# Performance work log

Hardware: AMD Instinct MI355X
Metric: run time of the kernel (lower is better)

The kernel has to match this reference:

```python
import jax, jax.numpy as jnp
import numpy as np

NUM_HEADS = 8
NUM_GROUPS = 32
EPS = 1e-5
RESCALE = 1.0


def setup_inputs() -> dict:
    key = jax.random.key(0)
    ks = jax.random.split(key, 7)
    b, c, h, w = 16, 512, 32, 32
    return {
        "x": jax.random.normal(ks[0], (b, c, h, w), jnp.float32),
        "norm_w": jax.random.normal(ks[1], (c,), jnp.float32),
        "norm_b": jax.random.normal(ks[2], (c,), jnp.float32),
        "qkv_w": jax.random.normal(ks[3], (3 * c, c), jnp.float32) * (c ** -0.5),
        "qkv_b": jax.random.normal(ks[4], (3 * c,), jnp.float32) * 0.02,
        "proj_w": jax.random.normal(ks[5], (c, c), jnp.float32) * (c ** -0.5),
        "proj_b": jax.random.normal(ks[6], (c,), jnp.float32) * 0.02,
    }


def _group_norm(x, w, b):
    # x: [B, C, L]
    B, C, L = x.shape
    g = x.reshape(B, NUM_GROUPS, (C // NUM_GROUPS) * L)
    mu = jnp.mean(g, axis=-1, keepdims=True)
    var = jnp.var(g, axis=-1, keepdims=True)
    g = (g - mu) * jax.lax.rsqrt(var + EPS)
    return g.reshape(B, C, L) * w[None, :, None] + b[None, :, None]


def reference(x, norm_w, norm_b, qkv_w, qkv_b, proj_w, proj_b):
    b, c, hh, ww = x.shape
    L = hh * ww
    H = NUM_HEADS
    ch = c // H  # head dim

    xr = x.reshape(b, c, L)
    hid = _group_norm(xr, norm_w, norm_b)

    # 1x1 conv1d == matmul over channel dim: [3c, c] @ [b, c, L]
    qkv = jnp.einsum('oc,bcl->bol', qkv_w, hid) + qkv_b[None, :, None]
    # torch: reshape(b*H, 3*ch, L).split(ch) -> per-head contiguous [q|k|v] blocks
    qkv = qkv.reshape(b, H, 3, ch, L)
    q, k, v = qkv[:, :, 0], qkv[:, :, 1], qkv[:, :, 2]  # [b, H, ch, L]

    scale = 1.0 / (ch ** 0.25)
    weight = jnp.einsum('bhct,bhcs->bhts', q * scale, k * scale)
    weight = jax.nn.softmax(weight.astype(jnp.float32), axis=-1).astype(weight.dtype)
    a = jnp.einsum('bhts,bhcs->bhct', weight, v)  # [b, H, ch, L]

    h = a.reshape(b, c, L)
    h = jnp.einsum('oc,bcl->bol', proj_w, h) + proj_b[None, :, None]
    h = h.reshape(b, c, hh, ww)
    return (x + h) / RESCALE
```

## Files before the change

### kernel.cpp

```cpp
#include <hip/hip_runtime.h>
#include <hip/hip_bf16.h>
#include <stdint.h>


using f32x4  = __attribute__((ext_vector_type(4))) float;
using bf16x8 = __attribute__((ext_vector_type(8))) __bf16;
using s8v    = __attribute__((ext_vector_type(8))) short;
using s4v    = __attribute__((ext_vector_type(4))) short;

__device__ __forceinline__ short f2bf(float f){
  union { float f; unsigned u; } c; c.f = f;
  unsigned r = (c.u + 0x7FFFu + ((c.u >> 16) & 1u)) >> 16;
  return (short)r;
}

__device__ __forceinline__ float exp2_fast(float x){
#if __has_builtin(__builtin_amdgcn_exp2f)
  return __builtin_amdgcn_exp2f(x);
#else
  return exp2f(x);
#endif
}

__device__ __forceinline__ void gl_lds16(const void* g, void* l){
  __builtin_amdgcn_global_load_lds((const __attribute__((address_space(1))) void*)g,
                                   (__attribute__((address_space(3))) void*)l, 16, 0, 0);
}

__global__ __launch_bounds__(256) void k_pre(const float* __restrict__ x,
                                             const float* __restrict__ w,
                                             const float* __restrict__ bia,
                                             short* __restrict__ hid,
                                             const float* __restrict__ qw,
                                             const float* __restrict__ pw,
                                             const float* __restrict__ qb,
                                             short* __restrict__ qwb,
                                             short* __restrict__ pwb,
                                             float* __restrict__ qbp){
  int bid = blockIdx.x;
  int tid = threadIdx.x;
  if (bid >= 512){
    int i = (bid - 512) * 256 + tid;
    if (i < 786432){
      int o = i >> 9, kk = i & 511;
      int h = o / 192, rem = o - h*192;
      int nr = (rem >> 6)*512 + h*64 + (rem & 63);
      qwb[nr*512 + kk] = f2bf(qw[i]);
    } else if (i < 1048576){
      int j = i - 786432;
      pwb[j] = f2bf(pw[j]);
    } else if (i < 1050112){
      int o = i - 1048576;
      int h = o / 192, rem = o - h*192;
      qbp[(rem >> 6)*512 + h*64 + (rem & 63)] = qb[o];
    }
    return;
  }
  int b = bid >> 5;
  int g = bid & 31;
  const float* xg = x + ((size_t)b*512 + g*16)*1024;
  int l0 = tid * 4;
  float v[16][4];
  float s1 = 0.f, s2 = 0.f;
  #pragma unroll
  for (int c = 0; c < 16; c++){
    f32x4 t = *(const f32x4*)(xg + c*1024 + l0);
    #pragma unroll
    for (int j = 0; j < 4; j++){ v[c][j] = t[j]; s1 += t[j]; s2 += t[j]*t[j]; }
  }
  #pragma unroll
  for (int m = 32; m; m >>= 1){ s1 += __shfl_xor(s1, m); s2 += __shfl_xor(s2, m); }
  __shared__ float r1[4], r2[4];
  int wv = tid >> 6, ln = tid & 63;
  if (ln == 0){ r1[wv] = s1; r2[wv] = s2; }
  __syncthreads();
  s1 = r1[0]+r1[1]+r1[2]+r1[3];
  s2 = r2[0]+r2[1]+r2[2]+r2[3];
  float mu = s1 * (1.f/16384.f);
  float var = s2 * (1.f/16384.f) - mu*mu;
  float rs = rsqrtf(var + 1e-5f);
  float ww[16], bb[16];
  #pragma unroll
  for (int c = 0; c < 16; c++){ ww[c] = w[g*16+c]*rs; bb[c] = bia[g*16+c]; }
  #pragma unroll
  for (int j = 0; j < 4; j++){
    short o[16];
    #pragma unroll
    for (int c = 0; c < 16; c++) o[c] = f2bf((v[c][j]-mu)*ww[c] + bb[c]);
    short* dst = hid + ((size_t)(b*1024 + l0 + j))*512 + g*16;
    *(s8v*)dst     = *(s8v*)o;
    *(s8v*)(dst+8) = *(s8v*)(o+8);
  }
}

__global__ __launch_bounds__(256) void k_gemmQ(
    const short* __restrict__ A, const short* __restrict__ Bm,
    const float* __restrict__ bias,
    short* __restrict__ q_t, short* __restrict__ k_t, short* __restrict__ v_t)
{
  __shared__ short Al[2][128*64];
  __shared__ short Bl[2][128*64];
  int id = blockIdx.x;
  int xcd = id & 7, ix = id >> 3;
  int mt = ix % 12, nt = ix / 12;
  int m0 = mt * 128;
  int n0 = (xcd + 8*nt) * 128;
  int tid = threadIdx.x;
  int lane = tid & 63;
  int wv = tid >> 6;
  int wr = wv >> 1, wc = wv & 1;
  int l15 = lane & 15, g = lane >> 4;
  f32x4 acc[4][4] = {};

  const short* srcp[8]; char* dstp[8];
  #pragma unroll
  for (int i = 0; i < 8; i++){
    int cc = wv*8 + i;
    if (cc < 16){
      int slot = cc*64 + lane;
      int row = slot >> 3, off = slot & 7;
      srcp[i] = A + (size_t)(m0+row)*512 + (off ^ (row&7))*8;
      dstp[i] = (char*)Al[0] + cc*1024;
    } else {
      int slot = (cc-16)*64 + lane;
      int row = slot >> 3, off = slot & 7;
      srcp[i] = Bm + (size_t)(n0+row)*512 + (off ^ (row&7))*8;
      dstp[i] = (char*)Bl[0] + (cc-16)*1024;
    }
  }

  auto STAGE = [&](int db, int t){
    #pragma unroll
    for (int i = 0; i < 8; i++)
      gl_lds16(srcp[i] + t*64, dstp[i] + db*16384);
  };

  auto COMPUTE = [&](int db){
    #pragma unroll
    for (int kk = 0; kk < 2; kk++){
      bf16x8 af[4], bf[4];
      #pragma unroll
      for (int m = 0; m < 4; m++){
        int row = wr*64 + m*16 + l15;
        int byte = row*128 + (((kk*64) + (g*16)) ^ ((row&7)<<4));
        af[m] = *(const bf16x8*)((char*)Al[db] + byte);
      }
      #pragma unroll
      for (int n = 0; n < 4; n++){
        int row = wc*64 + n*16 + l15;
        int byte = row*128 + (((kk*64) + (g*16)) ^ ((row&7)<<4));
        bf[n] = *(const bf16x8*)((char*)Bl[db] + byte);
      }
      __builtin_amdgcn_s_setprio(1);
      #pragma unroll
      for (int m = 0; m < 4; m++)
        #pragma unroll
        for (int n = 0; n < 4; n++)
          acc[m][n] = __builtin_amdgcn_mfma_f32_16x16x32_bf16(af[m], bf[n], acc[m][n], 0, 0, 0);
      __builtin_amdgcn_s_setprio(0);
    }
  };

  STAGE(0, 0);
  for (int t = 0; t < 8; t++){
    __syncthreads();
    if (t < 7) STAGE((t+1)&1, t+1);
    COMPUTE(t&1);
  }
  __syncthreads();

  int sel = m0 >> 9;
  if (sel < 2){
    const float sc = (sel == 0) ? 0.18033688011112042f : 1.0f;
    short* dstb = (sel == 0) ? q_t : k_t;
    #pragma unroll
    for (int m = 0; m < 4; m++){
      int ob = m0 + wr*64 + m*16 + (g<<2);
      int hh = (ob>>6)&7, c0 = ob&63;
      float bs[4];
      #pragma unroll
      for (int r = 0; r < 4; r++) bs[r] = bias[ob+r];
      #pragma unroll
      for (int n = 0; n < 4; n++){
        int nn = n0 + wc*64 + n*16 + l15;
        int bb = nn >> 10, ll = nn & 1023;
        int bh = bb*8 + hh;
        short o4[4];
        #pragma unroll
        for (int r = 0; r < 4; r++) o4[r] = f2bf((acc[m][n][r] + bs[r]) * sc);
        *(s4v*)(dstb + ((size_t)bh*1024 + ll)*64 + c0) = *(s4v*)o4;
      }
    }
  } else {
    short* Sc = (short*)Al;
    #pragma unroll
    for (int m = 0; m < 4; m++){
      int ob = m0 + wr*64 + m*16 + (g<<2);
      int h2 = (ob>>6)&1, cq = (ob>>4)&3;
      float bs[4];
      #pragma unroll
      for (int r = 0; r < 4; r++) bs[r] = bias[ob+r];
      #pragma unroll
      for (int n = 0; n < 4; n++){
        int nn = n0 + wc*64 + n*16 + l15;
        int sl = nn & 63, sreg = (nn>>6)&1;
        int ks2 = sl >> 5, gq = (sl>>2)&3, i2 = (sl&3) + 4*((sl>>4)&1);
        int base = (h2*2 + sreg)*4096 + (((ks2*4+gq)*4 + cq)*16 + (g<<2))*8 + i2;
        #pragma unroll
        for (int r = 0; r < 4; r++)
          Sc[base + r*8] = f2bf(acc[m][n][r] + bs[r]);
      }
    }
    __syncthreads();
    int b0  = n0 >> 10;
    int s64 = (n0 >> 6) & 15;
    int hb  = (m0 - 1024) >> 6;
    #pragma unroll
    for (int it = 0; it < 8; it++){
      int flat = it*2048 + tid*8;
      int h2 = flat >> 13, rem = flat & 8191, sreg = rem >> 12, off = rem & 4095;
      int bh = b0*8 + hb + h2;
      *(s8v*)(v_t + ((size_t)bh*16 + s64 + sreg)*4096 + off) = *(const s8v*)(Sc + flat);
    }
  }
}

__global__ __launch_bounds__(256) void k_gemmP(
    const short* __restrict__ A, const short* __restrict__ Bm,
    const float* __restrict__ bias, const float* __restrict__ xres,
    float* __restrict__ outp)
{
  __shared__ short Al[2][128*64];
  __shared__ short Bl[2][128*64];
  int id = blockIdx.x;
  int xcd = id & 7, ix = id >> 3;
  int mt = ix & 3, nt = ix >> 2;
  int m0 = mt * 128;
  int n0 = (xcd + 8*nt) * 128;
  int tid = threadIdx.x;
  int lane = tid & 63;
  int wv = tid >> 6;
  int wr = wv >> 1, wc = wv & 1;
  int l15 = lane & 15, g = lane >> 4;
  f32x4 acc[4][4] = {};

  const short* srcp[8]; char* dstp[8];
  #pragma unroll
  for (int i = 0; i < 8; i++){
    int cc = wv*8 + i;
    if (cc < 16){
      int slot = cc*64 + lane;
      int row = slot >> 3, off = slot & 7;
      srcp[i] = A + (size_t)(m0+row)*512 + (off ^ (row&7))*8;
      dstp[i] = (char*)Al[0] + cc*1024;
    } else {
      int slot = (cc-16)*64 + lane;
      int row = slot >> 3, off = slot & 7;
      srcp[i] = Bm + (size_t)(n0+row)*512 + (off ^ (row&7))*8;
      dstp[i] = (char*)Bl[0] + (cc-16)*1024;
    }
  }

  auto STAGE = [&](int db, int t){
    #pragma unroll
    for (int i = 0; i < 8; i++)
      gl_lds16(srcp[i] + t*64, dstp[i] + db*16384);
  };

  auto COMPUTE = [&](int db){
    #pragma unroll
    for (int kk = 0; kk < 2; kk++){
      bf16x8 af[4], bf[4];
      #pragma unroll
      for (int m = 0; m < 4; m++){
        int row = wr*64 + m*16 + l15;
        int byte = row*128 + (((kk*64) + (g*16)) ^ ((row&7)<<4));
        af[m] = *(const bf16x8*)((char*)Al[db] + byte);
      }
      #pragma unroll
      for (int n = 0; n < 4; n++){
        int row = wc*64 + n*16 + l15;
        int byte = row*128 + (((kk*64) + (g*16)) ^ ((row&7)<<4));
        bf[n] = *(const bf16x8*)((char*)Bl[db] + byte);
      }
      __builtin_amdgcn_s_setprio(1);
      #pragma unroll
      for (int m = 0; m < 4; m++)
        #pragma unroll
        for (int n = 0; n < 4; n++)
          acc[m][n] = __builtin_amdgcn_mfma_f32_16x16x32_bf16(af[m], bf[n], acc[m][n], 0, 0, 0);
      __builtin_amdgcn_s_setprio(0);
    }
  };

  STAGE(0, 0);
  for (int t = 0; t < 8; t++){
    __syncthreads();
    if (t < 7) STAGE((t+1)&1, t+1);
    COMPUTE(t&1);
  }

  #pragma unroll
  for (int m = 0; m < 4; m++){
    int ob = m0 + wr*64 + m*16 + (g<<2);
    float bs[4];
    #pragma unroll
    for (int r = 0; r < 4; r++) bs[r] = bias[ob+r];
    #pragma unroll
    for (int n = 0; n < 4; n++){
      int nn = n0 + wc*64 + n*16 + l15;
      int bb = nn >> 10, ll = nn & 1023;
      #pragma unroll
      for (int r = 0; r < 4; r++){
        size_t idx = ((size_t)bb*512 + ob + r)*1024 + ll;
        outp[idx] = xres[idx] + acc[m][n][r] + bs[r];
      }
    }
  }
}

__global__ __launch_bounds__(256, 4) void k_attn(
    const short* __restrict__ q_t, const short* __restrict__ k_t,
    const short* __restrict__ v_t, short* __restrict__ a_bt)
{
  __shared__ short Kh[4*2048];
  __shared__ short Vh[4*2048];
  int id = blockIdx.x;
  int xcd = id & 7, ix = id >> 3;
  int bh = xcd*16 + (ix >> 3);
  int qb = ix & 7;
  int bb = bh >> 3, hh = bh & 7;
  int tid = threadIdx.x;
  int lane = tid & 63;
  int wv = tid >> 6;
  int l15 = lane & 15, g = lane >> 4;

  bf16x8 qf[2][2];
  #pragma unroll
  for (int qt = 0; qt < 2; qt++){
    const short* qbase = q_t + ((size_t)bh*1024 + qb*128 + qt*64 + wv*16 + l15)*64 + g*8;
    qf[qt][0] = *(const bf16x8*)(qbase);
    qf[qt][1] = *(const bf16x8*)(qbase + 32);
  }
  asm volatile("" :: "v"(qf[0][0]), "v"(qf[0][1]), "v"(qf[1][0]), "v"(qf[1][1]));

  bf16x8 onesb;
  #pragma unroll
  for (int i = 0; i < 8; i++) onesb[i] = (__bf16)1.0f;

  f32x4 o[2][4] = {};
  f32x4 osum[2] = {};

  const short* sp[2]; char* dp[2];
  #pragma unroll
  for (int i = 0; i < 2; i++){
    int cc = wv*2 + i;
    if (cc < 4){
      int row = cc*8 + (lane>>3), slot = lane & 7;
      sp[i] = k_t + ((size_t)bh*1024 + row)*64 + (slot ^ (row&7))*8;
      dp[i] = (char*)Kh + cc*1024;
    } else {
      sp[i] = v_t + (size_t)bh*16*4096 + (cc-4)*512 + lane*8;
      dp[i] = (char*)Vh + (cc-4)*1024;
    }
  }
  auto STAGE = [&](int db, int h){
    #pragma unroll
    for (int i = 0; i < 2; i++)
      gl_lds16(sp[i] + h*2048, dp[i] + db*4096);
  };

  auto QK = [&](f32x4 (&scl)[2][2], int db){
    const char* Kb = (const char*)Kh + db*4096;
    #pragma unroll
    for (int qt = 0; qt < 2; qt++)
      #pragma unroll
      for (int jl = 0; jl < 2; jl++)
        scl[qt][jl] = f32x4{0.f, 0.f, 0.f, 0.f};
    #pragma unroll
    for (int jl = 0; jl < 2; jl++){
      int row = jl*16 + l15;
      int swz = (row&7)<<4;
      bf16x8 kf0 = *(const bf16x8*)(Kb + row*128 + ((g*16) ^ swz));
      bf16x8 kf1 = *(const bf16x8*)(Kb + row*128 + ((64 + g*16) ^ swz));
      __builtin_amdgcn_s_setprio(1);
      #pragma unroll
      for (int qt = 0; qt < 2; qt++){
        scl[qt][jl] = __builtin_amdgcn_mfma_f32_16x16x32_bf16(kf0, qf[qt][0], scl[qt][jl], 0, 0, 0);
        scl[qt][jl] = __builtin_amdgcn_mfma_f32_16x16x32_bf16(kf1, qf[qt][1], scl[qt][jl], 0, 0, 0);
      }
      __builtin_amdgcn_s_setprio(0);
    }
  };

  auto EXP_PV = [&](f32x4 (&scl)[2][2], int db){
    const char* Vb = (const char*)Vh + db*4096;
    bf16x8 pa[2];
    #pragma unroll
    for (int qt = 0; qt < 2; qt++){
      #pragma unroll
      for (int i2 = 0; i2 < 8; i2++)
        pa[qt][i2] = (__bf16)exp2_fast(scl[qt][i2>>2][i2&3]);
      osum[qt] = __builtin_amdgcn_mfma_f32_16x16x32_bf16(pa[qt], onesb, osum[qt], 0, 0, 0);
    }
    #pragma unroll
    for (int jd = 0; jd < 4; jd++){
      bf16x8 vbb = *(const bf16x8*)(Vb + (g*4+jd)*256 + l15*16);
      __builtin_amdgcn_s_setprio(1);
      #pragma unroll
      for (int qt = 0; qt < 2; qt++)
        o[qt][jd] = __builtin_amdgcn_mfma_f32_16x16x32_bf16(pa[qt], vbb, o[qt][jd], 0, 0, 0);
      __builtin_amdgcn_s_setprio(0);
    }
  };

  f32x4 sA[2][2], sB[2][2];

  STAGE(0, 0);
  STAGE(1, 1);
  asm volatile("s_waitcnt vmcnt(2)" ::: "memory");
  __builtin_amdgcn_s_barrier();
  __builtin_amdgcn_sched_barrier(0);
  QK(sA, 0);
  for (int h = 0; h < 30; h += 2){
    STAGE((h+2)&3, h+2);
    asm volatile("s_waitcnt vmcnt(2)" ::: "memory");
    __builtin_amdgcn_s_barrier();
    __builtin_amdgcn_sched_barrier(0);
    QK(sB, (h+1)&3);
    EXP_PV(sA, h&3);
    STAGE((h+3)&3, h+3);
    asm volatile("s_waitcnt vmcnt(2)" ::: "memory");
    __builtin_amdgcn_s_barrier();
    __builtin_amdgcn_sched_barrier(0);
    QK(sA, (h+2)&3);
    EXP_PV(sB, (h+1)&3);
  }
  asm volatile("s_waitcnt vmcnt(0)" ::: "memory");
  __builtin_amdgcn_s_barrier();
  __builtin_amdgcn_sched_barrier(0);
  QK(sB, 3);
  EXP_PV(sA, 2);
  EXP_PV(sB, 3);

  #pragma unroll
  for (int qt = 0; qt < 2; qt++){
    #pragma unroll
    for (int r = 0; r < 4; r++){
      float inv = 1.f / osum[qt][r];
      int qrow = qb*128 + qt*64 + wv*16 + g*4 + r;
      #pragma unroll
      for (int jd = 0; jd < 4; jd++)
        a_bt[((size_t)bb*1024 + qrow)*512 + hh*64 + jd*16 + l15] = f2bf(o[qt][jd][r] * inv);
    }
  }
}

extern "C" void kernel_launch(void* const* d_in, const int* in_sizes, int n_in,
                              void* d_out, int out_size, void* d_ws, size_t ws_size,
                              hipStream_t stream){
  const float* x  = (const float*)d_in[0];
  const float* nw = (const float*)d_in[1];
  const float* nb = (const float*)d_in[2];
  const float* qw = (const float*)d_in[3];
  const float* qb = (const float*)d_in[4];
  const float* pw = (const float*)d_in[5];
  const float* pb = (const float*)d_in[6];
  float* outp = (float*)d_out;

  char* ws = (char*)d_ws;
  short* hid  = (short*)(ws);
  short* qwb  = (short*)(ws + 16777216);
  short* pwb  = (short*)(ws + 18350080);
  short* q_t  = (short*)(ws + 18874368);
  short* k_t  = (short*)(ws + 35651584);
  short* v_t  = (short*)(ws + 52428800);
  short* a_bt = hid;
  float* qbp  = (float*)d_out;
  if (ws_size < 69206016) return;

  k_pre<<<4615, 256, 0, stream>>>(x, nw, nb, hid, qw, pw, qb, qwb, pwb, qbp);
  k_gemmQ<<<1536, 256, 0, stream>>>(qwb, hid, qbp, q_t, k_t, v_t);
  k_attn<<<1024, 256, 0, stream>>>(q_t, k_t, v_t, a_bt);
  k_gemmP<<<512, 256, 0, stream>>>(pwb, a_bt, pb, x, outp);
}
```

Baseline: 115.3 us.

## Switch attention kernel to 32x32x16 MFMA tiles with matching V layout

The attention kernel now uses 32x32x16 bf16 MFMA instructions instead of 16x16x32. Each wave handles 32 query rows against 32 keys per step, and the V staging layout written by the QKV GEMM epilogue is permuted to match the new operand fragment order. This is meant to cut the MFMA instruction count and the LDS fragment loads per step. In exchange it changes the accumulator register layout and the output row mapping, which risks register pressure and less even interleaving of exp and MFMA work.

```diff
diff --git a/kernel.cpp b/kernel.cpp
--- a/kernel.cpp
+++ b/kernel.cpp
@@ -4,6 +4,7 @@
 
 
 using f32x4  = __attribute__((ext_vector_type(4))) float;
+using f32x16 = __attribute__((ext_vector_type(16))) float;
 using bf16x8 = __attribute__((ext_vector_type(8))) __bf16;
 using s8v    = __attribute__((ext_vector_type(8))) short;
 using s4v    = __attribute__((ext_vector_type(4))) short;
@@ -196,7 +197,9 @@
     #pragma unroll
     for (int m = 0; m < 4; m++){
       int ob = m0 + wr*64 + m*16 + (g<<2);
-      int h2 = (ob>>6)&1, cq = (ob>>4)&3;
+      int h2 = (ob>>6)&1;
+      int dbase = ob & 63;
+      int dh = dbase >> 5, dl = dbase & 31;
       float bs[4];
       #pragma unroll
       for (int r = 0; r < 4; r++) bs[r] = bias[ob+r];
@@ -204,8 +207,10 @@
       for (int n = 0; n < 4; n++){
         int nn = n0 + wc*64 + n*16 + l15;
         int sl = nn & 63, sreg = (nn>>6)&1;
-        int ks2 = sl >> 5, gq = (sl>>2)&3, i2 = (sl&3) + 4*((sl>>4)&1);
-        int base = (h2*2 + sreg)*4096 + (((ks2*4+gq)*4 + cq)*16 + (g<<2))*8 + i2;
+        int ks2 = sl >> 5, s32 = sl & 31;
+        int c = s32 >> 4, s16 = s32 & 15;
+        int hc = (s16 >> 2) & 1, e = (s16 & 3) + 4*(s16 >> 3);
+        int base = (h2*2 + sreg)*4096 + ks2*2048 + (((c*2 + dh)*2 + hc)*32 + dl)*8 + e;
         #pragma unroll
         for (int r = 0; r < 4; r++)
           Sc[base + r*8] = f2bf(acc[m][n][r] + bs[r]);
@@ -333,23 +338,24 @@
   int tid = threadIdx.x;
   int lane = tid & 63;
   int wv = tid >> 6;
-  int l15 = lane & 15, g = lane >> 4;
-
-  bf16x8 qf[2][2];
-  #pragma unroll
-  for (int qt = 0; qt < 2; qt++){
-    const short* qbase = q_t + ((size_t)bh*1024 + qb*128 + qt*64 + wv*16 + l15)*64 + g*8;
-    qf[qt][0] = *(const bf16x8*)(qbase);
-    qf[qt][1] = *(const bf16x8*)(qbase + 32);
-  }
-  asm volatile("" :: "v"(qf[0][0]), "v"(qf[0][1]), "v"(qf[1][0]), "v"(qf[1][1]));
+  int l31 = lane & 31, h = lane >> 5;
+
+  bf16x8 qf[4];
+  {
+    const short* qbase = q_t + ((size_t)bh*1024 + qb*128 + wv*32 + l31)*64 + h*8;
+    qf[0] = *(const bf16x8*)(qbase);
+    qf[1] = *(const bf16x8*)(qbase + 16);
+    qf[2] = *(const bf16x8*)(qbase + 32);
+    qf[3] = *(const bf16x8*)(qbase + 48);
+  }
+  asm volatile("" :: "v"(qf[0]), "v"(qf[1]), "v"(qf[2]), "v"(qf[3]));
 
   bf16x8 onesb;
   #pragma unroll
   for (int i = 0; i < 8; i++) onesb[i] = (__bf16)1.0f;
 
-  f32x4 o[2][4] = {};
-  f32x4 osum[2] = {};
+  f32x16 o0 = {}, o1 = {};
+  f32x16 osum = {};
 
   const short* sp[2]; char* dp[2];
   #pragma unroll
@@ -364,57 +370,48 @@
       dp[i] = (char*)Vh + (cc-4)*1024;
     }
   }
-  auto STAGE = [&](int db, int h){
+  auto STAGE = [&](int db, int hf){
     #pragma unroll
     for (int i = 0; i < 2; i++)
-      gl_lds16(sp[i] + h*2048, dp[i] + db*4096);
-  };
-
-  auto QK = [&](f32x4 (&scl)[2][2], int db){
+      gl_lds16(sp[i] + hf*2048, dp[i] + db*4096);
+  };
+
+  auto QK = [&](f32x16& sc, int db){
     const char* Kb = (const char*)Kh + db*4096;
-    #pragma unroll
-    for (int qt = 0; qt < 2; qt++)
-      #pragma unroll
-      for (int jl = 0; jl < 2; jl++)
-        scl[qt][jl] = f32x4{0.f, 0.f, 0.f, 0.f};
-    #pragma unroll
-    for (int jl = 0; jl < 2; jl++){
-      int row = jl*16 + l15;
-      int swz = (row&7)<<4;
-      bf16x8 kf0 = *(const bf16x8*)(Kb + row*128 + ((g*16) ^ swz));
-      bf16x8 kf1 = *(const bf16x8*)(Kb + row*128 + ((64 + g*16) ^ swz));
-      __builtin_amdgcn_s_setprio(1);
-      #pragma unroll
-      for (int qt = 0; qt < 2; qt++){
-        scl[qt][jl] = __builtin_amdgcn_mfma_f32_16x16x32_bf16(kf0, qf[qt][0], scl[qt][jl], 0, 0, 0);
-        scl[qt][jl] = __builtin_amdgcn_mfma_f32_16x16x32_bf16(kf1, qf[qt][1], scl[qt][jl], 0, 0, 0);
-      }
-      __builtin_amdgcn_s_setprio(0);
-    }
-  };
-
-  auto EXP_PV = [&](f32x4 (&scl)[2][2], int db){
+    sc = f32x16{};
+    __builtin_amdgcn_s_setprio(1);
+    #pragma unroll
+    for (int d0 = 0; d0 < 4; d0++){
+      int byte = l31*128 + (((d0*32) + h*16) ^ ((l31&7)<<4));
+      bf16x8 kf = *(const bf16x8*)(Kb + byte);
+      sc = __builtin_amdgcn_mfma_f32_32x32x16_bf16(kf, qf[d0], sc, 0, 0, 0);
+    }
+    __builtin_amdgcn_s_setprio(0);
+  };
+
+  auto EXP_PV = [&](f32x16& sc, int db){
     const char* Vb = (const char*)Vh + db*4096;
-    bf16x8 pa[2];
-    #pragma unroll
-    for (int qt = 0; qt < 2; qt++){
-      #pragma unroll
-      for (int i2 = 0; i2 < 8; i2++)
-        pa[qt][i2] = (__bf16)exp2_fast(scl[qt][i2>>2][i2&3]);
-      osum[qt] = __builtin_amdgcn_mfma_f32_16x16x32_bf16(pa[qt], onesb, osum[qt], 0, 0, 0);
-    }
-    #pragma unroll
-    for (int jd = 0; jd < 4; jd++){
-      bf16x8 vbb = *(const bf16x8*)(Vb + (g*4+jd)*256 + l15*16);
-      __builtin_amdgcn_s_setprio(1);
-      #pragma unroll
-      for (int qt = 0; qt < 2; qt++)
-        o[qt][jd] = __builtin_amdgcn_mfma_f32_16x16x32_bf16(pa[qt], vbb, o[qt][jd], 0, 0, 0);
-      __builtin_amdgcn_s_setprio(0);
-    }
-  };
-
-  f32x4 sA[2][2], sB[2][2];
+    bf16x8 pa0, pa1;
+    #pragma unroll
+    for (int e = 0; e < 8; e++){
+      pa0[e] = (__bf16)exp2_fast(sc[e]);
+      pa1[e] = (__bf16)exp2_fast(sc[8+e]);
+    }
+    osum = __builtin_amdgcn_mfma_f32_32x32x16_bf16(pa0, onesb, osum, 0, 0, 0);
+    osum = __builtin_amdgcn_mfma_f32_32x32x16_bf16(pa1, onesb, osum, 0, 0, 0);
+    bf16x8 v00 = *(const bf16x8*)(Vb + (0*2+h)*512 + l31*16);
+    bf16x8 v01 = *(const bf16x8*)(Vb + (2   +h)*512 + l31*16);
+    bf16x8 v10 = *(const bf16x8*)(Vb + (4   +h)*512 + l31*16);
+    bf16x8 v11 = *(const bf16x8*)(Vb + (6   +h)*512 + l31*16);
+    __builtin_amdgcn_s_setprio(1);
+    o0 = __builtin_amdgcn_mfma_f32_32x32x16_bf16(pa0, v00, o0, 0, 0, 0);
+    o0 = __builtin_amdgcn_mfma_f32_32x32x16_bf16(pa1, v10, o0, 0, 0, 0);
+    o1 = __builtin_amdgcn_mfma_f32_32x32x16_bf16(pa0, v01, o1, 0, 0, 0);
+    o1 = __builtin_amdgcn_mfma_f32_32x32x16_bf16(pa1, v11, o1, 0, 0, 0);
+    __builtin_amdgcn_s_setprio(0);
+  };
+
+  f32x16 sA, sB;
 
   STAGE(0, 0);
   STAGE(1, 1);
@@ -422,19 +419,19 @@
   __builtin_amdgcn_s_barrier();
   __builtin_amdgcn_sched_barrier(0);
   QK(sA, 0);
-  for (int h = 0; h < 30; h += 2){
-    STAGE((h+2)&3, h+2);
+  for (int hf = 0; hf < 30; hf += 2){
+    STAGE((hf+2)&3, hf+2);
     asm volatile("s_waitcnt vmcnt(2)" ::: "memory");
     __builtin_amdgcn_s_barrier();
     __builtin_amdgcn_sched_barrier(0);
-    QK(sB, (h+1)&3);
-    EXP_PV(sA, h&3);
-    STAGE((h+3)&3, h+3);
+    QK(sB, (hf+1)&3);
+    EXP_PV(sA, hf&3);
+    STAGE((hf+3)&3, hf+3);
     asm volatile("s_waitcnt vmcnt(2)" ::: "memory");
     __builtin_amdgcn_s_barrier();
     __builtin_amdgcn_sched_barrier(0);
-    QK(sA, (h+2)&3);
-    EXP_PV(sB, (h+1)&3);
+    QK(sA, (hf+2)&3);
+    EXP_PV(sB, (hf+1)&3);
   }
   asm volatile("s_waitcnt vmcnt(0)" ::: "memory");
   __builtin_amdgcn_s_barrier();
@@ -444,15 +441,12 @@
   EXP_PV(sB, 3);
 
   #pragma unroll
-  for (int qt = 0; qt < 2; qt++){
-    #pragma unroll
-    for (int r = 0; r < 4; r++){
-      float inv = 1.f / osum[qt][r];
-      int qrow = qb*128 + qt*64 + wv*16 + g*4 + r;
-      #pragma unroll
-      for (int jd = 0; jd < 4; jd++)
-        a_bt[((size_t)bb*1024 + qrow)*512 + hh*64 + jd*16 + l15] = f2bf(o[qt][jd][r] * inv);
-    }
+  for (int r = 0; r < 16; r++){
+    float inv = 1.f / osum[r];
+    int qrow = qb*128 + wv*32 + (r&3) + 8*(r>>2) + 4*h;
+    size_t base = ((size_t)bb*1024 + qrow)*512 + hh*64;
+    a_bt[base + l31]      = f2bf(o0[r] * inv);
+    a_bt[base + 32 + l31] = f2bf(o1[r] * inv);
   }
 }
 
```

Result: slower. 119.0 us (+3.3%).

## Triple-buffer GEMM K-loop with 32-wide K tiles and explicit vmcnt waits

Applied to the files above, without the earlier changes.

Both the QKV and projection GEMM kernels move from a double-buffered loop over 64-wide K tiles to a triple-buffered loop over 32-wide K tiles. Loads run two stages ahead, and each step waits with s_waitcnt vmcnt instead of a full __syncthreads. The LDS swizzle is reworked for 64-byte rows. The aim is to hide global-to-LDS latency better while keeping the LDS footprint the same (48KB), at the cost of twice as many barrier iterations and less MFMA work per step. The waitcnt counts rely on how the compiler places the async loads.

```diff
diff --git a/kernel.cpp b/kernel.cpp
--- a/kernel.cpp
+++ b/kernel.cpp
@@ -98,8 +98,7 @@
     const float* __restrict__ bias,
     short* __restrict__ q_t, short* __restrict__ k_t, short* __restrict__ v_t)
 {
-  __shared__ short Al[2][128*64];
-  __shared__ short Bl[2][128*64];
+  __shared__ short Lds[3*8192];
   int id = blockIdx.x;
   int xcd = id & 7, ix = id >> 3;
   int mt = ix % 12, nt = ix / 12;
@@ -112,60 +111,60 @@
   int l15 = lane & 15, g = lane >> 4;
   f32x4 acc[4][4] = {};
 
-  const short* srcp[8]; char* dstp[8];
-  #pragma unroll
-  for (int i = 0; i < 8; i++){
-    int cc = wv*8 + i;
-    if (cc < 16){
-      int slot = cc*64 + lane;
-      int row = slot >> 3, off = slot & 7;
-      srcp[i] = A + (size_t)(m0+row)*512 + (off ^ (row&7))*8;
-      dstp[i] = (char*)Al[0] + cc*1024;
+  const short* srcp[4]; char* dstp[4];
+  #pragma unroll
+  for (int i = 0; i < 4; i++){
+    int cc = wv*4 + i;
+    int c2 = cc & 7;
+    int row = c2*16 + (lane>>2), slot = lane & 3;
+    if (cc < 8){
+      srcp[i] = A + (size_t)(m0+row)*512 + ((slot ^ ((row>>1)&3))*8);
+      dstp[i] = (char*)Lds + c2*1024;
     } else {
-      int slot = (cc-16)*64 + lane;
-      int row = slot >> 3, off = slot & 7;
-      srcp[i] = Bm + (size_t)(n0+row)*512 + (off ^ (row&7))*8;
-      dstp[i] = (char*)Bl[0] + (cc-16)*1024;
-    }
-  }
-
-  auto STAGE = [&](int db, int t){
-    #pragma unroll
-    for (int i = 0; i < 8; i++)
-      gl_lds16(srcp[i] + t*64, dstp[i] + db*16384);
-  };
-
-  auto COMPUTE = [&](int db){
-    #pragma unroll
-    for (int kk = 0; kk < 2; kk++){
-      bf16x8 af[4], bf[4];
-      #pragma unroll
-      for (int m = 0; m < 4; m++){
-        int row = wr*64 + m*16 + l15;
-        int byte = row*128 + (((kk*64) + (g*16)) ^ ((row&7)<<4));
-        af[m] = *(const bf16x8*)((char*)Al[db] + byte);
-      }
-      #pragma unroll
-      for (int n = 0; n < 4; n++){
-        int row = wc*64 + n*16 + l15;
-        int byte = row*128 + (((kk*64) + (g*16)) ^ ((row&7)<<4));
-        bf[n] = *(const bf16x8*)((char*)Bl[db] + byte);
-      }
-      __builtin_amdgcn_s_setprio(1);
-      #pragma unroll
-      for (int m = 0; m < 4; m++)
-        #pragma unroll
-        for (int n = 0; n < 4; n++)
-          acc[m][n] = __builtin_amdgcn_mfma_f32_16x16x32_bf16(af[m], bf[n], acc[m][n], 0, 0, 0);
-      __builtin_amdgcn_s_setprio(0);
-    }
+      srcp[i] = Bm + (size_t)(n0+row)*512 + ((slot ^ ((row>>1)&3))*8);
+      dstp[i] = (char*)Lds + 8192 + c2*1024;
+    }
+  }
+
+  auto STAGE = [&](int b, int t){
+    #pragma unroll
+    for (int i = 0; i < 4; i++)
+      gl_lds16(srcp[i] + t*32, dstp[i] + b*16384);
+  };
+
+  auto COMPUTE = [&](int b){
+    const char* Ab = (const char*)Lds + b*16384;
+    const char* Bb = Ab + 8192;
+    bf16x8 af[4], bf[4];
+    #pragma unroll
+    for (int m = 0; m < 4; m++){
+      int row = wr*64 + m*16 + l15;
+      af[m] = *(const bf16x8*)(Ab + row*64 + ((g*16) ^ (((row>>1)&3)<<4)));
+    }
+    #pragma unroll
+    for (int n = 0; n < 4; n++){
+      int row = wc*64 + n*16 + l15;
+      bf[n] = *(const bf16x8*)(Bb + row*64 + ((g*16) ^ (((row>>1)&3)<<4)));
+    }
+    __builtin_amdgcn_s_setprio(1);
+    #pragma unroll
+    for (int m = 0; m < 4; m++)
+      #pragma unroll
+      for (int n = 0; n < 4; n++)
+        acc[m][n] = __builtin_amdgcn_mfma_f32_16x16x32_bf16(af[m], bf[n], acc[m][n], 0, 0, 0);
+    __builtin_amdgcn_s_setprio(0);
   };
 
   STAGE(0, 0);
-  for (int t = 0; t < 8; t++){
-    __syncthreads();
-    if (t < 7) STAGE((t+1)&1, t+1);
-    COMPUTE(t&1);
+  STAGE(1, 1);
+  #pragma unroll
+  for (int t = 0; t < 16; t++){
+    if (t < 15) asm volatile("s_waitcnt vmcnt(4)" ::: "memory");
+    else        asm volatile("s_waitcnt vmcnt(0)" ::: "memory");
+    __builtin_amdgcn_s_barrier();
+    __builtin_amdgcn_sched_barrier(0);
+    if (t < 14) STAGE((t+2)%3, t+2);
+    COMPUTE(t%3);
   }
   __syncthreads();
 
@@ -192,7 +191,7 @@
       }
     }
   } else {
-    short* Sc = (short*)Al;
+    short* Sc = Lds;
     #pragma unroll
     for (int m = 0; m < 4; m++){
       int ob = m0 + wr*64 + m*16 + (g<<2);
@@ -230,8 +229,7 @@
     const float* __restrict__ bias, const float* __restrict__ xres,
     float* __restrict__ outp)
 {
-  __shared__ short Al[2][128*64];
-  __shared__ short Bl[2][128*64];
+  __shared__ short Lds[3*8192];
   int id = blockIdx.x;
   int xcd = id & 7, ix = id >> 3;
   int mt = ix & 3, nt = ix >> 2;
@@ -244,60 +242,60 @@
   int l15 = lane & 15, g = lane >> 4;
   f32x4 acc[4][4] = {};
 
-  const short* srcp[8]; char* dstp[8];
-  #pragma unroll
-  for (int i = 0; i < 8; i++){
-    int cc = wv*8 + i;
-    if (cc < 16){
-      int slot = cc*64 + lane;
-      int row = slot >> 3, off = slot & 7;
-      srcp[i] = A + (size_t)(m0+row)*512 + (off ^ (row&7))*8;
-      dstp[i] = (char*)Al[0] + cc*1024;
+  const short* srcp[4]; char* dstp[4];
+  #pragma unroll
+  for (int i = 0; i < 4; i++){
+    int cc = wv*4 + i;
+    int c2 = cc & 7;
+    int row = c2*16 + (lane>>2), slot = lane & 3;
+    if (cc < 8){
+      srcp[i] = A + (size_t)(m0+row)*512 + ((slot ^ ((row>>1)&3))*8);
+      dstp[i] = (char*)Lds + c2*1024;
     } else {
-      int slot = (cc-16)*64 + lane;
-      int row = slot >> 3, off = slot & 7;
-      srcp[i] = Bm + (size_t)(n0+row)*512 + (off ^ (row&7))*8;
-      dstp[i] = (char*)Bl[0] + (cc-16)*1024;
-    }
-  }
-
-  auto STAGE = [&](int db, int t){
-    #pragma unroll
-    for (int i = 0; i < 8; i++)
-      gl_lds16(srcp[i] + t*64, dstp[i] + db*16384);
-  };
-
-  auto COMPUTE = [&](int db){
-    #pragma unroll
-    for (int kk = 0; kk < 2; kk++){
-      bf16x8 af[4], bf[4];
-      #pragma unroll
-      for (int m = 0; m < 4; m++){
-        int row = wr*64 + m*16 + l15;
-        int byte = row*128 + (((kk*64) + (g*16)) ^ ((row&7)<<4));
-        af[m] = *(const bf16x8*)((char*)Al[db] + byte);
-      }
-      #pragma unroll
-      for (int n = 0; n < 4; n++){
-        int row = wc*64 + n*16 + l15;
-        int byte = row*128 + (((kk*64) + (g*16)) ^ ((row&7)<<4));
-        bf[n] = *(const bf16x8*)((char*)Bl[db] + byte);
-      }
-      __builtin_amdgcn_s_setprio(1);
-      #pragma unroll
-      for (int m = 0; m < 4; m++)
-        #pragma unroll
-        for (int n = 0; n < 4; n++)
-          acc[m][n] = __builtin_amdgcn_mfma_f32_16x16x32_bf16(af[m], bf[n], acc[m][n], 0, 0, 0);
-      __builtin_amdgcn_s_setprio(0);
-    }
+      srcp[i] = Bm + (size_t)(n0+row)*512 + ((slot ^ ((row>>1)&3))*8);
+      dstp[i] = (char*)Lds + 8192 + c2*1024;
+    }
+  }
+
+  auto STAGE = [&](int b, int t){
+    #pragma unroll
+    for (int i = 0; i < 4; i++)
+      gl_lds16(srcp[i] + t*32, dstp[i] + b*16384);
+  };
+
+  auto COMPUTE = [&](int b){
+    const char* Ab = (const char*)Lds + b*16384;
+    const char* Bb = Ab + 8192;
+    bf16x8 af[4], bf[4];
+    #pragma unroll
+    for (int m = 0; m < 4; m++){
+      int row = wr*64 + m*16 + l15;
+      af[m] = *(const bf16x8*)(Ab + row*64 + ((g*16) ^ (((row>>1)&3)<<4)));
+    }
+    #pragma unroll
+    for (int n = 0; n < 4; n++){
+      int row = wc*64 + n*16 + l15;
+      bf[n] = *(const bf16x8*)(Bb + row*64 + ((g*16) ^ (((row>>1)&3)<<4)));
+    }
+    __builtin_amdgcn_s_setprio(1);
+    #pragma unroll
+    for (int m = 0; m < 4; m++)
+      #pragma unroll
+      for (int n = 0; n < 4; n++)
+        acc[m][n] = __builtin_amdgcn_mfma_f32_16x16x32_bf16(af[m], bf[n], acc[m][n], 0, 0, 0);
+    __builtin_amdgcn_s_setprio(0);
   };
 
   STAGE(0, 0);
-  for (int t = 0; t < 8; t++){
-    __syncthreads();
-    if (t < 7) STAGE((t+1)&1, t+1);
-    COMPUTE(t&1);
+  STAGE(1, 1);
+  #pragma unroll
+  for (int t = 0; t < 16; t++){
+    if (t < 15) asm volatile("s_waitcnt vmcnt(4)" ::: "memory");
+    else        asm volatile("s_waitcnt vmcnt(0)" ::: "memory");
+    __builtin_amdgcn_s_barrier();
+    __builtin_amdgcn_sched_barrier(0);
+    if (t < 14) STAGE((t+2)%3, t+2);
+    COMPUTE(t%3);
   }
 
   #pragma unroll
```

Measured after the change: 117.9 us. 1.02x slower.

## Load K/V fragments directly from global memory in attention kernel, drop LDS staging

Applied to the files above, without the earlier changes.

The attention kernel no longer stages K and V tiles through shared memory with async global-to-LDS copies, a 4-deep ring buffer and per-tile barriers. Each wave now loads its K and V MFMA fragments straight from global memory into registers inside a plain loop unrolled by 2. The aim is to remove barrier and LDS round-trip overhead and free LDS for more resident blocks. The cost is that the four waves of a block each load the same K/V data redundantly, with no explicit prefetch to hide latency.

```diff
diff --git a/kernel.cpp b/kernel.cpp
--- a/kernel.cpp
+++ b/kernel.cpp
@@ -319,12 +319,10 @@
   }
 }
 
-__global__ __launch_bounds__(256, 4) void k_attn(
+__global__ __launch_bounds__(256) void k_attn(
     const short* __restrict__ q_t, const short* __restrict__ k_t,
     const short* __restrict__ v_t, short* __restrict__ a_bt)
 {
-  __shared__ short Kh[4*2048];
-  __shared__ short Vh[4*2048];
   int id = blockIdx.x;
   int xcd = id & 7, ix = id >> 3;
   int bh = xcd*16 + (ix >> 3);
@@ -342,7 +340,6 @@
     qf[qt][0] = *(const bf16x8*)(qbase);
     qf[qt][1] = *(const bf16x8*)(qbase + 32);
   }
-  asm volatile("" :: "v"(qf[0][0]), "v"(qf[0][1]), "v"(qf[1][0]), "v"(qf[1][1]));
 
   bf16x8 onesb;
   #pragma unroll
@@ -351,50 +348,36 @@
   f32x4 o[2][4] = {};
   f32x4 osum[2] = {};
 
-  const short* sp[2]; char* dp[2];
-  #pragma unroll
-  for (int i = 0; i < 2; i++){
-    int cc = wv*2 + i;
-    if (cc < 4){
-      int row = cc*8 + (lane>>3), slot = lane & 7;
-      sp[i] = k_t + ((size_t)bh*1024 + row)*64 + (slot ^ (row&7))*8;
-      dp[i] = (char*)Kh + cc*1024;
-    } else {
-      sp[i] = v_t + (size_t)bh*16*4096 + (cc-4)*512 + lane*8;
-      dp[i] = (char*)Vh + (cc-4)*1024;
-    }
-  }
-  auto STAGE = [&](int db, int h){
-    #pragma unroll
-    for (int i = 0; i < 2; i++)
-      gl_lds16(sp[i] + h*2048, dp[i] + db*4096);
-  };
-
-  auto QK = [&](f32x4 (&scl)[2][2], int db){
-    const char* Kb = (const char*)Kh + db*4096;
-    #pragma unroll
-    for (int qt = 0; qt < 2; qt++)
-      #pragma unroll
-      for (int jl = 0; jl < 2; jl++)
-        scl[qt][jl] = f32x4{0.f, 0.f, 0.f, 0.f};
-    #pragma unroll
-    for (int jl = 0; jl < 2; jl++){
-      int row = jl*16 + l15;
-      int swz = (row&7)<<4;
-      bf16x8 kf0 = *(const bf16x8*)(Kb + row*128 + ((g*16) ^ swz));
-      bf16x8 kf1 = *(const bf16x8*)(Kb + row*128 + ((64 + g*16) ^ swz));
-      __builtin_amdgcn_s_setprio(1);
-      #pragma unroll
-      for (int qt = 0; qt < 2; qt++){
-        scl[qt][jl] = __builtin_amdgcn_mfma_f32_16x16x32_bf16(kf0, qf[qt][0], scl[qt][jl], 0, 0, 0);
-        scl[qt][jl] = __builtin_amdgcn_mfma_f32_16x16x32_bf16(kf1, qf[qt][1], scl[qt][jl], 0, 0, 0);
-      }
-      __builtin_amdgcn_s_setprio(0);
-    }
-  };
-
-  auto EXP_PV = [&](f32x4 (&scl)[2][2], int db){
-    const char* Vb = (const char*)Vh + db*4096;
+  const short* kb = k_t + ((size_t)bh*1024 + l15)*64 + g*8;
+  const short* vb = v_t + (size_t)bh*16*4096 + g*512 + l15*8;
+
+  #pragma unroll 2
+  for (int h = 0; h < 32; h++){
+    bf16x8 k00 = *(const bf16x8*)(kb + (h*32     )*64);
+    bf16x8 k01 = *(const bf16x8*)(kb + (h*32     )*64 + 32);
+    bf16x8 k10 = *(const bf16x8*)(kb + (h*32 + 16)*64);
+    bf16x8 k11 = *(const bf16x8*)(kb + (h*32 + 16)*64 + 32);
+    f32x4 scl[2][2];
+    #pragma unroll
+    for (int qt = 0; qt < 2; qt++){
+      scl[qt][0] = f32x4{0.f,0.f,0.f,0.f};
+      scl[qt][1] = f32x4{0.f,0.f,0.f,0.f};
+    }
+    __builtin_amdgcn_s_setprio(1);
+    #pragma unroll
+    for (int qt = 0; qt < 2; qt++){
+      scl[qt][0] = __builtin_amdgcn_mfma_f32_16x16x32_bf16(k00, qf[qt][0], scl[qt][0], 0, 0, 0);
+      scl[qt][0] = __builtin_amdgcn_mfma_f32_16x16x32_bf16(k01, qf[qt][1], scl[qt][0], 0, 0, 0);
+      scl[qt][1] = __builtin_amdgcn_mfma_f32_16x16x32_bf16(k10, qf[qt][0], scl[qt][1], 0, 0, 0);
+      scl[qt][1] = __builtin_amdgcn_mfma_f32_16x16x32_bf16(k11, qf[qt][1], scl[qt][1], 0, 0, 0);
+    }
+    __builtin_amdgcn_s_setprio(0);
+
+    bf16x8 vb0 = *(const bf16x8*)(vb + h*2048      );
+    bf16x8 vb1 = *(const bf16x8*)(vb + h*2048 + 128);
+    bf16x8 vb2 = *(const bf16x8*)(vb + h*2048 + 256);
+    bf16x8 vb3 = *(const bf16x8*)(vb + h*2048 + 384);
+
     bf16x8 pa[2];
     #pragma unroll
     for (int qt = 0; qt < 2; qt++){
@@ -403,45 +386,16 @@
         pa[qt][i2] = (__bf16)exp2_fast(scl[qt][i2>>2][i2&3]);
       osum[qt] = __builtin_amdgcn_mfma_f32_16x16x32_bf16(pa[qt], onesb, osum[qt], 0, 0, 0);
     }
-    #pragma unroll
-    for (int jd = 0; jd < 4; jd++){
-      bf16x8 vbb = *(const bf16x8*)(Vb + (g*4+jd)*256 + l15*16);
-      __builtin_amdgcn_s_setprio(1);
-      #pragma unroll
-      for (int qt = 0; qt < 2; qt++)
-        o[qt][jd] = __builtin_amdgcn_mfma_f32_16x16x32_bf16(pa[qt], vbb, o[qt][jd], 0, 0, 0);
-      __builtin_amdgcn_s_setprio(0);
-    }
-  };
-
-  f32x4 sA[2][2], sB[2][2];
-
-  STAGE(0, 0);
-  STAGE(1, 1);
-  asm volatile("s_waitcnt vmcnt(2)" ::: "memory");
-  __builtin_amdgcn_s_barrier();
-  __builtin_amdgcn_sched_barrier(0);
-  QK(sA, 0);
-  for (int h = 0; h < 30; h += 2){
-    STAGE((h+2)&3, h+2);
-    asm volatile("s_waitcnt vmcnt(2)" ::: "memory");
-    __builtin_amdgcn_s_barrier();
-    __builtin_amdgcn_sched_barrier(0);
-    QK(sB, (h+1)&3);
-    EXP_PV(sA, h&3);
-    STAGE((h+3)&3, h+3);
-    asm volatile("s_waitcnt vmcnt(2)" ::: "memory");
-    __builtin_amdgcn_s_barrier();
-    __builtin_amdgcn_sched_barrier(0);
-    QK(sA, (h+2)&3);
-    EXP_PV(sB, (h+1)&3);
-  }
-  asm volatile("s_waitcnt vmcnt(0)" ::: "memory");
-  __builtin_amdgcn_s_barrier();
-  __builtin_amdgcn_sched_barrier(0);
-  QK(sB, 3);
-  EXP_PV(sA, 2);
-  EXP_PV(sB, 3);
+    __builtin_amdgcn_s_setprio(1);
+    #pragma unroll
+    for (int qt = 0; qt < 2; qt++){
+      o[qt][0] = __builtin_amdgcn_mfma_f32_16x16x32_bf16(pa[qt], vb0, o[qt][0], 0, 0, 0);
+      o[qt][1] = __builtin_amdgcn_mfma_f32_16x16x32_bf16(pa[qt], vb1, o[qt][1], 0, 0, 0);
+      o[qt][2] = __builtin_amdgcn_mfma_f32_16x16x32_bf16(pa[qt], vb2, o[qt][2], 0, 0, 0);
+      o[qt][3] = __builtin_amdgcn_mfma_f32_16x16x32_bf16(pa[qt], vb3, o[qt][3], 0, 0, 0);
+    }
+    __builtin_amdgcn_s_setprio(0);
+  }
 
   #pragma unroll
   for (int qt = 0; qt < 2; qt++){
```

Measured after the change: 172.5 us. 1.5x slower.
